# Performance work log

Hardware: AMD Instinct MI355X
Metric: run time of the kernel (lower is better)

Reference implementation:

```python
import jax, jax.numpy as jnp
import numpy as np

IN_SIZE = 128
H_UNITS = 256
REC_MAX = min(25.0, 1.0 / float(np.sqrt(H_UNITS)))  # clip bound for recurrent kernels


def setup_inputs() -> dict:
    key = jax.random.key(0)
    ks = jax.random.split(key, 8)
    B, T, D, U = 64, 4096, IN_SIZE, H_UNITS
    xs = jax.random.normal(ks[0], (B, T, D), dtype=jnp.float32)
    # Original code inits input kernels/biases to zeros (degenerate); use small
    # random values so the baseline exercises nontrivial math (same formula).
    We = jax.random.normal(ks[1], (U, D), dtype=jnp.float32) * 0.02
    be = jnp.zeros((U,), dtype=jnp.float32)
    ue = jax.random.uniform(ks[2], (U,), minval=-REC_MAX, maxval=REC_MAX, dtype=jnp.float32)
    Wd = jax.random.normal(ks[3], (U, D), dtype=jnp.float32) * 0.02
    bd = jnp.zeros((U,), dtype=jnp.float32)
    ud = jax.random.uniform(ks[4], (U,), minval=-REC_MAX, maxval=REC_MAX, dtype=jnp.float32)
    lim = 1.0 / float(np.sqrt(U))  # torch.nn.Linear default init bound
    Wo = jax.random.uniform(ks[5], (D, U), minval=-lim, maxval=lim, dtype=jnp.float32)
    bo = jax.random.uniform(ks[6], (D,), minval=-lim, maxval=lim, dtype=jnp.float32)
    return {"xs": xs, "We": We, "be": be, "ue": ue, "Wd": Wd, "bd": bd, "ud": ud, "Wo": Wo, "bo": bo}


def reference(xs, We, be, ue, Wd, bd, ud, Wo, bo):
    B, T, D = xs.shape
    ue_c = jnp.clip(ue, -REC_MAX, REC_MAX)
    ud_c = jnp.clip(ud, -REC_MAX, REC_MAX)
    # IndRNN.forward never updates self.h, so the encoder hidden state is zeros
    # at every timestep; the encoder loop reduces to its last iteration:
    h = jax.nn.relu(xs[:, -1] @ We.T + be + ue_c * 0.0)  # [B, U]
    # ys[0]: readout of the (fixed) decoder hidden state
    out0 = h @ Wo.T + bo  # [B, D]
    loss = (xs[:, -1] - out0) ** 2  # [B, D]
    # train_step: decoder h stays fixed at encoder h for every timestep ->
    # all T-1 steps vectorize over time.
    dec_h = jax.nn.relu(jnp.einsum('btd,ud->btu', xs[:, 1:], Wd) + bd + ud_c * h[:, None, :])  # [B,T-1,U]
    outs = jnp.einsum('btu,du->btd', dec_h, Wo) + bo  # [B,T-1,D]
    loss = loss + jnp.sum((xs[:, :-1] - outs) ** 2, axis=1)  # sum over reversed(range(1,T))
    loss = loss / T
    return jnp.sum(loss) / B
```

## Files before the change

kernel.cpp:

```cpp
#include <hip/hip_runtime.h>

#define T_LEN 4096
#define D_IN 128
#define U_H 256
#define REC_MAXV 0.0625f

typedef __attribute__((ext_vector_type(4))) float f32x4;
typedef __attribute__((ext_vector_type(16))) float f32x16;
typedef __attribute__((ext_vector_type(2))) int int2v;
typedef long long i64;

template <bool HI>
__device__ __forceinline__ int pk8(float a, float b, int old) {
    return __builtin_amdgcn_cvt_pk_fp8_f32(a, b, old, HI);
}

__global__ void k_h(const float* __restrict__ xs, const float* __restrict__ We,
                    const float* __restrict__ be, float* __restrict__ h) {
    int b = blockIdx.x, u = threadIdx.x;
    const f32x4* xr = (const f32x4*)(xs + ((size_t)b * T_LEN + (T_LEN - 1)) * D_IN);
    const f32x4* wr = (const f32x4*)(We + (size_t)u * D_IN);
    float s = 0.f;
#pragma unroll
    for (int i = 0; i < 32; ++i) {
        f32x4 a = xr[i], w = wr[i];
        s += a[0]*w[0] + a[1]*w[1] + a[2]*w[2] + a[3]*w[3];
    }
    s += be[u];
    h[b * U_H + u] = fmaxf(s, 0.f);
}

__global__ void k_prep(const float* __restrict__ Wd, const float* __restrict__ Wo,
                       const float* __restrict__ bd, const float* __restrict__ ud,
                       const float* __restrict__ bo, const float* __restrict__ hbuf,
                       float* __restrict__ budR, float* __restrict__ boR,
                       char* __restrict__ WF8, float* __restrict__ loss) {
    int gid = blockIdx.x * 256 + threadIdx.x;
    int u = gid & 255, b = gid >> 8;
    float udc = fminf(fmaxf(ud[u], -REC_MAXV), REC_MAXV);
    float budv = bd[u] + udc * hbuf[gid];
    {
        int r = u & 31;
        budR[(b << 8) + ((u >> 5) << 5) + (((r >> 2) & 1) << 4) + ((r >> 3) << 2) + (r & 3)] = budv;
    }
    if (gid == 0) *loss = 0.f;
    if (gid < 128) {
        int r = gid & 31;
        boR[((gid >> 5) << 5) + (((r >> 2) & 1) << 4) + ((r >> 3) << 2) + (r & 3)] = bo[gid];
    }
    if (gid < 4096) {
        int f = gid >> 6, l = gid & 63;
        int ut = f >> 3, ks = f & 7;
        const float* src = Wd + (size_t)(ut * 32 + (l & 31)) * D_IN + ks * 16 + (l >> 5) * 8;
        int lo = pk8<false>(src[0], src[1], 0); lo = pk8<true>(src[2], src[3], lo);
        int hh = pk8<false>(src[4], src[5], 0); hh = pk8<true>(src[6], src[7], hh);
        *(int2v*)(WF8 + (size_t)gid * 8) = (int2v){lo, hh};
    } else if (gid < 8192) {
        int g = gid - 4096;
        int f = g >> 6, l = g & 63;
        int uk = f >> 2, dt = f & 3;
        const float* src = Wo + (size_t)(dt * 32 + (l & 31)) * U_H + uk * 16 + (l >> 5) * 8;
        int lo = pk8<false>(src[0], src[1], 0); lo = pk8<true>(src[2], src[3], lo);
        int hh = pk8<false>(src[4], src[5], 0); hh = pk8<true>(src[6], src[7], hh);
        *(int2v*)(WF8 + 32768 + (size_t)g * 8) = (int2v){lo, hh};
    }
}

__global__ void k_loss0(const float* __restrict__ xs, const float* __restrict__ hbuf,
                        const float* __restrict__ Wo, const float* __restrict__ bo,
                        float* __restrict__ loss) {
    int b = blockIdx.x, d = threadIdx.x;
    const f32x4* hr = (const f32x4*)(hbuf + b * U_H);
    const f32x4* wr = (const f32x4*)(Wo + (size_t)d * U_H);
    float s = 0.f;
#pragma unroll
    for (int i = 0; i < 64; ++i) {
        f32x4 a = hr[i], w = wr[i];
        s += a[0]*w[0] + a[1]*w[1] + a[2]*w[2] + a[3]*w[3];
    }
    s += bo[d];
    float x = xs[((size_t)b * T_LEN + T_LEN - 1) * D_IN + d];
    float diff = x - s;
    float v = diff * diff;
#pragma unroll
    for (int o = 32; o > 0; o >>= 1) v += __shfl_down(v, o);
    if ((threadIdx.x & 63) == 0) atomicAdd(loss, v * (1.f / 262144.f));
}

__device__ __forceinline__ void ph1(const char* lds, const float* budL,
                                    int lane, int hi, int ut,
                                    i64 x0, i64 x1, i64 x2, i64 x3,
                                    i64 x4, i64 x5, i64 x6, i64 x7,
                                    i64& dlo, i64& dhi) {
    f32x16 ca, cb;
#pragma unroll
    for (int i = 0; i < 16; ++i) { ca[i] = 0.f; cb[i] = 0.f; }
    const int base = (ut * 8) << 9;
    ca = __builtin_amdgcn_mfma_f32_32x32x16_fp8_fp8(*(const i64*)(lds + base + (0<<9) + (lane<<3)), x0, ca, 0,0,0);
    cb = __builtin_amdgcn_mfma_f32_32x32x16_fp8_fp8(*(const i64*)(lds + base + (1<<9) + (lane<<3)), x1, cb, 0,0,0);
    ca = __builtin_amdgcn_mfma_f32_32x32x16_fp8_fp8(*(const i64*)(lds + base + (2<<9) + (lane<<3)), x2, ca, 0,0,0);
    cb = __builtin_amdgcn_mfma_f32_32x32x16_fp8_fp8(*(const i64*)(lds + base + (3<<9) + (lane<<3)), x3, cb, 0,0,0);
    ca = __builtin_amdgcn_mfma_f32_32x32x16_fp8_fp8(*(const i64*)(lds + base + (4<<9) + (lane<<3)), x4, ca, 0,0,0);
    cb = __builtin_amdgcn_mfma_f32_32x32x16_fp8_fp8(*(const i64*)(lds + base + (5<<9) + (lane<<3)), x5, cb, 0,0,0);
    ca = __builtin_amdgcn_mfma_f32_32x32x16_fp8_fp8(*(const i64*)(lds + base + (6<<9) + (lane<<3)), x6, ca, 0,0,0);
    cb = __builtin_amdgcn_mfma_f32_32x32x16_fp8_fp8(*(const i64*)(lds + base + (7<<9) + (lane<<3)), x7, cb, 0,0,0);
    const float* bp = budL + ut * 32 + hi * 16;
    f32x16 c;
#pragma unroll
    for (int q = 0; q < 4; ++q) {
        f32x4 bq = *(const f32x4*)(bp + q * 4);
#pragma unroll
        for (int j = 0; j < 4; ++j)
            c[q * 4 + j] = fmaxf(ca[q * 4 + j] + cb[q * 4 + j] + bq[j], 0.f);
    }
    int d0 = pk8<false>(c[0],  c[1],  0); d0 = pk8<true>(c[2],  c[3],  d0);
    int d1 = pk8<false>(c[4],  c[5],  0); d1 = pk8<true>(c[6],  c[7],  d1);
    int d2 = pk8<false>(c[8],  c[9],  0); d2 = pk8<true>(c[10], c[11], d2);
    int d3 = pk8<false>(c[12], c[13], 0); d3 = pk8<true>(c[14], c[15], d3);
    int2v s = __builtin_amdgcn_permlane32_swap(d0, d1, false, false);
    int2v t = __builtin_amdgcn_permlane32_swap(d2, d3, false, false);
    dlo = __builtin_bit_cast(i64, s);
    dhi = __builtin_bit_cast(i64, t);
    __builtin_amdgcn_sched_barrier(0);
}

__device__ __forceinline__ void ph2(const char* lds, int lane, int dc, int uk,
                                    i64 db, f32x16& oA, f32x16& oB) {
    i64 w0 = *(const i64*)(lds + 32768 + ((uk * 4 + dc * 2 + 0) << 9) + (lane << 3));
    i64 w1 = *(const i64*)(lds + 32768 + ((uk * 4 + dc * 2 + 1) << 9) + (lane << 3));
    oA = __builtin_amdgcn_mfma_f32_32x32x16_fp8_fp8(w0, db, oA, 0, 0, 0);
    oB = __builtin_amdgcn_mfma_f32_32x32x16_fp8_fp8(w1, db, oB, 0, 0, 0);
}

__global__ __launch_bounds__(512, 2) void k_main(
        const float* __restrict__ xs, const float* __restrict__ budR,
        const float* __restrict__ boR, const char* __restrict__ WF8,
        float* __restrict__ part) {
    __shared__ __align__(16) char lds[67136];
    const int tid = threadIdx.x;

    for (int i = tid; i < 4096; i += 512)
        ((f32x4*)lds)[i] = ((const f32x4*)WF8)[i];
    const int b = blockIdx.x >> 4;
    if (tid < 64) ((f32x4*)(lds + 65536))[tid] = ((const f32x4*)(budR + b * 256))[tid];
    else if (tid < 96) ((f32x4*)(lds + 66560))[tid - 64] = ((const f32x4*)boR)[tid - 64];
    __syncthreads();

    const int wave = tid >> 6, lane = tid & 63;
    const int m = lane & 31, hi = lane >> 5;
    const float* xsb = xs + ((size_t)b << 19);
    const float* budL = (const float*)(lds + 65536);
    const float* boL  = (const float*)(lds + 66560);
    float* wsumf = (float*)(lds + 67072);

    const int tile = blockIdx.x * 8 + wave;
    const int t0 = (tile & 127) << 5;

    const float* xrow = xsb + (size_t)(t0 + m) * 128 + hi * 8;
    i64 x0, x1, x2, x3, x4, x5, x6, x7;
    {
#define LDX(KS, XV)                                                      \
        {   f32x4 v0 = *(const f32x4*)(xrow + KS * 16);                  \
            f32x4 v1 = *(const f32x4*)(xrow + KS * 16 + 4);              \
            int lo = pk8<false>(v0[0], v0[1], 0); lo = pk8<true>(v0[2], v0[3], lo); \
            int hh = pk8<false>(v1[0], v1[1], 0); hh = pk8<true>(v1[2], v1[3], hh); \
            XV = __builtin_bit_cast(i64, (int2v){lo, hh}); }
        LDX(0, x0) LDX(1, x1) LDX(2, x2) LDX(3, x3)
        LDX(4, x4) LDX(5, x5) LDX(6, x6) LDX(7, x7)
#undef LDX
    }

    i64 d0a, d0b, d1a, d1b, d2a, d2b, d3a, d3b;
    i64 d4a, d4b, d5a, d5b, d6a, d6b, d7a, d7b;
    ph1(lds, budL, lane, hi, 0, x0,x1,x2,x3,x4,x5,x6,x7, d0a, d0b);
    ph1(lds, budL, lane, hi, 1, x0,x1,x2,x3,x4,x5,x6,x7, d1a, d1b);
    ph1(lds, budL, lane, hi, 2, x0,x1,x2,x3,x4,x5,x6,x7, d2a, d2b);
    ph1(lds, budL, lane, hi, 3, x0,x1,x2,x3,x4,x5,x6,x7, d3a, d3b);
    ph1(lds, budL, lane, hi, 4, x0,x1,x2,x3,x4,x5,x6,x7, d4a, d4b);
    ph1(lds, budL, lane, hi, 5, x0,x1,x2,x3,x4,x5,x6,x7, d5a, d5b);
    ph1(lds, budL, lane, hi, 6, x0,x1,x2,x3,x4,x5,x6,x7, d6a, d6b);
    ph1(lds, budL, lane, hi, 7, x0,x1,x2,x3,x4,x5,x6,x7, d7a, d7b);

    const int t = t0 + m;
    const float sel = (t > 0) ? 1.f : 0.f;
    const float* trow = xsb + (size_t)((t > 0) ? t - 1 : 0) * 128;
    float lacc = 0.f;

#pragma unroll
    for (int dc = 0; dc < 2; ++dc) {
        f32x16 o0a, o0b, o1a, o1b;
#pragma unroll
        for (int i = 0; i < 16; ++i) { o0a[i] = 0.f; o0b[i] = 0.f; o1a[i] = 0.f; o1b[i] = 0.f; }
        ph2(lds, lane, dc,  0, d0a, o0a, o1a);
        ph2(lds, lane, dc,  1, d0b, o0b, o1b);
        ph2(lds, lane, dc,  2, d1a, o0a, o1a);
        ph2(lds, lane, dc,  3, d1b, o0b, o1b);
        ph2(lds, lane, dc,  4, d2a, o0a, o1a);
        ph2(lds, lane, dc,  5, d2b, o0b, o1b);
        ph2(lds, lane, dc,  6, d3a, o0a, o1a);
        ph2(lds, lane, dc,  7, d3b, o0b, o1b);
        ph2(lds, lane, dc,  8, d4a, o0a, o1a);
        ph2(lds, lane, dc,  9, d4b, o0b, o1b);
        ph2(lds, lane, dc, 10, d5a, o0a, o1a);
        ph2(lds, lane, dc, 11, d5b, o0b, o1b);
        ph2(lds, lane, dc, 12, d6a, o0a, o1a);
        ph2(lds, lane, dc, 13, d6b, o0b, o1b);
        ph2(lds, lane, dc, 14, d7a, o0a, o1a);
        ph2(lds, lane, dc, 15, d7b, o0b, o1b);
        __builtin_amdgcn_sched_barrier(0);
#pragma unroll
        for (int half = 0; half < 2; ++half) {
            const int dt = dc * 2 + half;
#pragma unroll
            for (int q = 0; q < 4; ++q) {
                f32x4 bv = *(const f32x4*)(boL + dt * 32 + hi * 16 + q * 4);
                f32x4 tg = *(const f32x4*)(trow + dt * 32 + q * 8 + hi * 4);
#pragma unroll
                for (int j = 0; j < 4; ++j) {
                    float ov = (half ? o1a[q * 4 + j] + o1b[q * 4 + j]
                                     : o0a[q * 4 + j] + o0b[q * 4 + j]) + bv[j];
                    float diff = tg[j] - ov;
                    lacc += sel * diff * diff;
                }
            }
        }
    }

#pragma unroll
    for (int o = 32; o > 0; o >>= 1) lacc += __shfl_down(lacc, o);
    if (lane == 0) wsumf[wave] = lacc;
    __syncthreads();
    if (tid == 0) {
        float s = 0.f;
#pragma unroll
        for (int i = 0; i < 8; ++i) s += wsumf[i];
        part[blockIdx.x] = s;
    }
}

__global__ void k_final(const float* __restrict__ part, float* __restrict__ loss) {
    __shared__ float ws[16];
    const int tid = threadIdx.x;
    float v = part[tid];
#pragma unroll
    for (int o = 32; o > 0; o >>= 1) v += __shfl_down(v, o);
    if ((tid & 63) == 0) ws[tid >> 6] = v;
    __syncthreads();
    if (tid == 0) {
        float s = 0.f;
#pragma unroll
        for (int i = 0; i < 16; ++i) s += ws[i];
        atomicAdd(loss, s * (1.f / 262144.f));
    }
}

extern "C" void kernel_launch(void* const* d_in, const int* in_sizes, int n_in,
                              void* d_out, int out_size, void* d_ws, size_t ws_size,
                              hipStream_t stream) {
    const float* xs = (const float*)d_in[0];
    const float* We = (const float*)d_in[1];
    const float* be = (const float*)d_in[2];
    const float* Wd = (const float*)d_in[4];
    const float* bd = (const float*)d_in[5];
    const float* ud = (const float*)d_in[6];
    const float* Wo = (const float*)d_in[7];
    const float* bo = (const float*)d_in[8];
    float* loss = (float*)d_out;

    char* ws = (char*)d_ws;
    float* h    = (float*)(ws);
    float* budR = (float*)(ws + 65536);
    char*  WF8  = (char*)(ws + 131072);
    float* boR  = (float*)(ws + 196608);
    float* part = (float*)(ws + 197120);

    k_h<<<64, 256, 0, stream>>>(xs, We, be, h);
    k_prep<<<64, 256, 0, stream>>>(Wd, Wo, bd, ud, bo, h, budR, boR, WF8, loss);
    k_loss0<<<64, 128, 0, stream>>>(xs, h, Wo, bo, loss);
    k_main<<<1024, 512, 0, stream>>>(xs, budR, boR, WF8, part);
    k_final<<<1, 1024, 0, stream>>>(part, loss);
}
```

Before: 66.45 us.

## Fuse preprocessing kernels and double main block size to 1024 threads

Merges the encoder, weight/bias prep and initial-loss kernels into one kernel, with h kept in shared memory, which removes two launches and a global round trip for h. The loss0 partials now go to a workspace array that the final kernel sums and writes directly, so the atomic adds and the separate loss zeroing are gone. The main kernel now uses 1024-thread blocks covering 16 tiles, so the FP8 weight staging into LDS happens half as often. The trade is fewer resident blocks per CU and a longer block-wide barrier.

```diff
diff --git a/kernel.cpp b/kernel.cpp
--- a/kernel.cpp
+++ b/kernel.cpp
@@ -15,9 +15,21 @@
     return __builtin_amdgcn_cvt_pk_fp8_f32(a, b, old, HI);
 }
 
-__global__ void k_h(const float* __restrict__ xs, const float* __restrict__ We,
-                    const float* __restrict__ be, float* __restrict__ h) {
-    int b = blockIdx.x, u = threadIdx.x;
+__device__ __forceinline__ int reord32(int u) {
+    int r = u & 31;
+    return ((u >> 5) << 5) + (((r >> 2) & 1) << 4) + ((r >> 3) << 2) + (r & 3);
+}
+
+__global__ void k_pre(const float* __restrict__ xs, const float* __restrict__ We,
+                      const float* __restrict__ be, const float* __restrict__ Wd,
+                      const float* __restrict__ bd, const float* __restrict__ ud,
+                      const float* __restrict__ Wo, const float* __restrict__ bo,
+                      float* __restrict__ budR, float* __restrict__ boR,
+                      char* __restrict__ WF8, float* __restrict__ part2) {
+    __shared__ __align__(16) float hL[256];
+    __shared__ float red[2];
+    const int b = blockIdx.x, u = threadIdx.x;
+
     const f32x4* xr = (const f32x4*)(xs + ((size_t)b * T_LEN + (T_LEN - 1)) * D_IN);
     const f32x4* wr = (const f32x4*)(We + (size_t)u * D_IN);
     float s = 0.f;
@@ -27,27 +39,15 @@
         s += a[0]*w[0] + a[1]*w[1] + a[2]*w[2] + a[3]*w[3];
     }
     s += be[u];
-    h[b * U_H + u] = fmaxf(s, 0.f);
-}
-
-__global__ void k_prep(const float* __restrict__ Wd, const float* __restrict__ Wo,
-                       const float* __restrict__ bd, const float* __restrict__ ud,
-                       const float* __restrict__ bo, const float* __restrict__ hbuf,
-                       float* __restrict__ budR, float* __restrict__ boR,
-                       char* __restrict__ WF8, float* __restrict__ loss) {
-    int gid = blockIdx.x * 256 + threadIdx.x;
-    int u = gid & 255, b = gid >> 8;
+    s = fmaxf(s, 0.f);
+    hL[u] = s;
+
     float udc = fminf(fmaxf(ud[u], -REC_MAXV), REC_MAXV);
-    float budv = bd[u] + udc * hbuf[gid];
-    {
-        int r = u & 31;
-        budR[(b << 8) + ((u >> 5) << 5) + (((r >> 2) & 1) << 4) + ((r >> 3) << 2) + (r & 3)] = budv;
-    }
-    if (gid == 0) *loss = 0.f;
-    if (gid < 128) {
-        int r = gid & 31;
-        boR[((gid >> 5) << 5) + (((r >> 2) & 1) << 4) + ((r >> 3) << 2) + (r & 3)] = bo[gid];
-    }
+    budR[(b << 8) + reord32(u)] = bd[u] + udc * s;
+
+    if (b == 0 && u < 128) boR[reord32(u)] = bo[u];
+
+    int gid = b * 256 + u;
     if (gid < 4096) {
         int f = gid >> 6, l = gid & 63;
         int ut = f >> 3, ks = f & 7;
@@ -64,27 +64,29 @@
         int hh = pk8<false>(src[4], src[5], 0); hh = pk8<true>(src[6], src[7], hh);
         *(int2v*)(WF8 + 32768 + (size_t)g * 8) = (int2v){lo, hh};
     }
-}
-
-__global__ void k_loss0(const float* __restrict__ xs, const float* __restrict__ hbuf,
-                        const float* __restrict__ Wo, const float* __restrict__ bo,
-                        float* __restrict__ loss) {
-    int b = blockIdx.x, d = threadIdx.x;
-    const f32x4* hr = (const f32x4*)(hbuf + b * U_H);
-    const f32x4* wr = (const f32x4*)(Wo + (size_t)d * U_H);
-    float s = 0.f;
-#pragma unroll
-    for (int i = 0; i < 64; ++i) {
-        f32x4 a = hr[i], w = wr[i];
-        s += a[0]*w[0] + a[1]*w[1] + a[2]*w[2] + a[3]*w[3];
-    }
-    s += bo[d];
-    float x = xs[((size_t)b * T_LEN + T_LEN - 1) * D_IN + d];
-    float diff = x - s;
-    float v = diff * diff;
+    __syncthreads();
+
+    float v = 0.f;
+    if (u < 128) {
+        const f32x4* hr = (const f32x4*)hL;
+        const f32x4* wo = (const f32x4*)(Wo + (size_t)u * U_H);
+        float s2 = 0.f;
+#pragma unroll
+        for (int i = 0; i < 64; ++i) {
+            f32x4 a = hr[i], w = wo[i];
+            s2 += a[0]*w[0] + a[1]*w[1] + a[2]*w[2] + a[3]*w[3];
+        }
+        s2 += bo[u];
+        float x = xs[((size_t)b * T_LEN + T_LEN - 1) * D_IN + u];
+        float diff = x - s2;
+        v = diff * diff;
+    }
 #pragma unroll
     for (int o = 32; o > 0; o >>= 1) v += __shfl_down(v, o);
-    if ((threadIdx.x & 63) == 0) atomicAdd(loss, v * (1.f / 262144.f));
+    if (u == 0) red[0] = v;
+    if (u == 64) red[1] = v;
+    __syncthreads();
+    if (u == 0) part2[b] = red[0] + red[1];
 }
 
 __device__ __forceinline__ void ph1(const char* lds, const float* budL,
@@ -132,16 +134,16 @@
     oB = __builtin_amdgcn_mfma_f32_32x32x16_fp8_fp8(w1, db, oB, 0, 0, 0);
 }
 
-__global__ __launch_bounds__(512, 2) void k_main(
+__global__ __launch_bounds__(1024, 4) void k_main(
         const float* __restrict__ xs, const float* __restrict__ budR,
         const float* __restrict__ boR, const char* __restrict__ WF8,
         float* __restrict__ part) {
-    __shared__ __align__(16) char lds[67136];
+    __shared__ __align__(16) char lds[67200];
     const int tid = threadIdx.x;
 
-    for (int i = tid; i < 4096; i += 512)
+    for (int i = tid; i < 4096; i += 1024)
         ((f32x4*)lds)[i] = ((const f32x4*)WF8)[i];
-    const int b = blockIdx.x >> 4;
+    const int b = blockIdx.x >> 3;
     if (tid < 64) ((f32x4*)(lds + 65536))[tid] = ((const f32x4*)(budR + b * 256))[tid];
     else if (tid < 96) ((f32x4*)(lds + 66560))[tid - 64] = ((const f32x4*)boR)[tid - 64];
     __syncthreads();
@@ -153,7 +155,7 @@
     const float* boL  = (const float*)(lds + 66560);
     float* wsumf = (float*)(lds + 67072);
 
-    const int tile = blockIdx.x * 8 + wave;
+    const int tile = blockIdx.x * 16 + wave;
     const int t0 = (tile & 127) << 5;
 
     const float* xrow = xsb + (size_t)(t0 + m) * 128 + hi * 8;
@@ -233,15 +235,17 @@
     if (tid == 0) {
         float s = 0.f;
 #pragma unroll
-        for (int i = 0; i < 8; ++i) s += wsumf[i];
+        for (int i = 0; i < 16; ++i) s += wsumf[i];
         part[blockIdx.x] = s;
     }
 }
 
-__global__ void k_final(const float* __restrict__ part, float* __restrict__ loss) {
+__global__ void k_final(const float* __restrict__ part, const float* __restrict__ part2,
+                        float* __restrict__ loss) {
     __shared__ float ws[16];
     const int tid = threadIdx.x;
-    float v = part[tid];
+    float v = (tid < 512) ? part[tid] : 0.f;
+    if (tid < 64) v += part2[tid];
 #pragma unroll
     for (int o = 32; o > 0; o >>= 1) v += __shfl_down(v, o);
     if ((tid & 63) == 0) ws[tid >> 6] = v;
@@ -250,7 +254,7 @@
         float s = 0.f;
 #pragma unroll
         for (int i = 0; i < 16; ++i) s += ws[i];
-        atomicAdd(loss, s * (1.f / 262144.f));
+        *loss = s * (1.f / 262144.f);
     }
 }
 
@@ -268,15 +272,14 @@
     float* loss = (float*)d_out;
 
     char* ws = (char*)d_ws;
-    float* h    = (float*)(ws);
-    float* budR = (float*)(ws + 65536);
-    char*  WF8  = (char*)(ws + 131072);
-    float* boR  = (float*)(ws + 196608);
-    float* part = (float*)(ws + 197120);
-
-    k_h<<<64, 256, 0, stream>>>(xs, We, be, h);
-    k_prep<<<64, 256, 0, stream>>>(Wd, Wo, bd, ud, bo, h, budR, boR, WF8, loss);
-    k_loss0<<<64, 128, 0, stream>>>(xs, h, Wo, bo, loss);
-    k_main<<<1024, 512, 0, stream>>>(xs, budR, boR, WF8, part);
-    k_final<<<1, 1024, 0, stream>>>(part, loss);
-}
+    float* budR  = (float*)(ws);
+    char*  WF8   = (char*)(ws + 65536);
+    float* boR   = (float*)(ws + 131072);
+    float* part  = (float*)(ws + 131584);
+    float* part2 = (float*)(ws + 133632);
+
+    k_pre<<<64, 256, 0, stream>>>(xs, We, be, Wd, bd, ud, Wo, bo,
+                                  budR, boR, WF8, part2);
+    k_main<<<512, 1024, 0, stream>>>(xs, budR, boR, WF8, part);
+    k_final<<<1, 1024, 0, stream>>>(part, part2, loss);
+}
```

Measured after the change: 63.74 us. 1.04x faster.
